# Performance work log

Measured on AMD Instinct MI355X. Metric: run time of the kernel, lower is better.

Reference implementation:

```python
import jax, jax.numpy as jnp
import numpy as np

B, M, HWIN = 1024, 5, 25          # batch, encoder window, decoder horizon
SH, SW, HID = 64, 128, 256        # saliency map H/W, hidden size
SAL = SH * SW


def setup_inputs() -> dict:
    key = jax.random.key(0)
    ks = jax.random.split(key, 32)
    s = 0.02
    W = lambda k, shp: (jax.random.normal(k, shp, jnp.float32) * s)
    inp = {
        "enc_pos": jax.random.normal(ks[0], (B, M, 3), jnp.float32),
        "enc_sal": jax.random.uniform(ks[1], (B, M, SH, SW), jnp.float32),
        "dec_pos": jax.random.normal(ks[2], (B, 1, 3), jnp.float32),
        "dec_sal": jax.random.uniform(ks[3], (B, HWIN, SH, SW), jnp.float32),
        # fc_pos_enc / fc_sal_enc
        "Wpe": W(ks[4], (3, HID)),    "bpe": W(ks[5], (HID,)),
        "Wse": W(ks[6], (SAL, HID)),  "bse": W(ks[7], (HID,)),
        # fuse_1_enc LSTM (gate order i,f,g,o like torch)
        "Wih_e": W(ks[8], (2 * HID, 4 * HID)), "Whh_e": W(ks[9], (HID, 4 * HID)),
        "bih_e": W(ks[10], (4 * HID,)),        "bhh_e": W(ks[11], (4 * HID,)),
        # fuse_1_dec LSTM
        "Wih_d": W(ks[12], (2 * HID, 4 * HID)), "Whh_d": W(ks[13], (HID, 4 * HID)),
        "bih_d": W(ks[14], (4 * HID,)),         "bhh_d": W(ks[15], (4 * HID,)),
        # fc_pos_dec / fc_sal_dec
        "Wpd": W(ks[16], (3, HID)),   "bpd": W(ks[17], (HID,)),
        "Wsd": W(ks[18], (SAL, HID)), "bsd": W(ks[19], (HID,)),
        # fuse_2 and fc_layer_out
        "W2": W(ks[20], (HID, HID)),  "b2": W(ks[21], (HID,)),
        "Wo": W(ks[22], (HID, 3)),    "bo": W(ks[23], (3,)),
    }
    return inp


def _lstm_cell(h, c, x, Wih, Whh, b):
    g = x @ Wih + h @ Whh + b                     # [B, 4H]
    i, f, gg, o = jnp.split(g, 4, axis=-1)        # torch gate order i,f,g,o
    c = jax.nn.sigmoid(f) * c + jax.nn.sigmoid(i) * jnp.tanh(gg)
    h = jax.nn.sigmoid(o) * jnp.tanh(c)
    return h, c


def reference(enc_pos, enc_sal, dec_pos, dec_sal,
              Wpe, bpe, Wse, bse, Wih_e, Whh_e, bih_e, bhh_e,
              Wih_d, Whh_d, bih_d, bhh_d, Wpd, bpd, Wsd, bsd,
              W2, b2, Wo, bo):
    b = enc_pos.shape[0]
    hid = Whh_e.shape[0]
    # ---- encoder: per-timestep linear features, then LSTM over M steps ----
    sal_e = enc_sal.reshape(b, enc_sal.shape[1], -1) @ Wse + bse   # [B,M,H]
    pos_e = enc_pos @ Wpe + bpe                                     # [B,M,H]
    x_e = jnp.concatenate([sal_e, pos_e], axis=-1)                  # [B,M,2H]
    be = bih_e + bhh_e

    h0 = jnp.zeros((b, hid), enc_pos.dtype)
    c0 = jnp.zeros((b, hid), enc_pos.dtype)

    def enc_step(carry, xt):
        h, c = carry
        h, c = _lstm_cell(h, c, xt, Wih_e, Whh_e, be)
        return (h, c), None

    (h, c), _ = jax.lax.scan(enc_step, (h0, c0), jnp.swapaxes(x_e, 0, 1))

    sal_d = dec_sal.reshape(b, dec_sal.shape[1], -1) @ Wsd + bsd    # [B,Hw,H]
    bd = bih_d + bhh_d

    def dec_step(carry, sal_t):
        h, c, pos = carry                       # pos: [B,3]
        pf = pos @ Wpd + bpd                    # fc_pos_dec
        x = jnp.concatenate([sal_t, pf], axis=-1)
        h, c = _lstm_cell(h, c, x, Wih_d, Whh_d, bd)
        delta = (h @ W2 + b2) @ Wo + bo         # fuse_2 -> fc_layer_out
        newpos = pos + delta                    # toPosition: add delta,
        newpos = newpos / jnp.linalg.norm(newpos, axis=-1, keepdims=True)
        return (h, c, newpos), newpos

    pos0 = dec_pos[:, 0, :]
    _, outs = jax.lax.scan(dec_step, (h, c, pos0), jnp.swapaxes(sal_d, 0, 1))
    return jnp.swapaxes(outs, 0, 1)             # [B, H_WINDOW, 3]
```

## Files before the change

kernel.cpp:

```cpp
#include <hip/hip_runtime.h>

typedef _Float16 f16;
typedef _Float16 f16x4 __attribute__((ext_vector_type(4)));
typedef _Float16 f16x8 __attribute__((ext_vector_type(8)));
typedef float    f32x4 __attribute__((ext_vector_type(4)));
typedef int      i32x4 __attribute__((ext_vector_type(4)));
typedef unsigned int u32;

#define MFMA16(a,b,c) __builtin_amdgcn_mfma_f32_16x16x32_f16((a),(b),(c),0,0,0)
#define MFMAI8(a,b,c) __builtin_amdgcn_mfma_i32_16x16x64_i8((a),(b),(c),0,0,0)

typedef __attribute__((address_space(1))) const u32 gu32;
typedef __attribute__((address_space(3))) u32 lu32;

static __device__ __forceinline__ float frcp(float x){ float r; asm("v_rcp_f32 %0, %1" : "=v"(r) : "v"(x)); return r; }
static __device__ __forceinline__ float frsq(float x){ float r; asm("v_rsq_f32 %0, %1" : "=v"(r) : "v"(x)); return r; }
static __device__ __forceinline__ float sigm(float x){ return frcp(1.0f + __expf(-x)); }
static __device__ __forceinline__ float tanh_(float x){ return 1.0f - 2.0f*frcp(1.0f + __expf(2.0f*x)); }

static __device__ __forceinline__ void bar_lgkm(){
  asm volatile("s_waitcnt lgkmcnt(0)" ::: "memory");
  __builtin_amdgcn_s_barrier();
  asm volatile("" ::: "memory");
}
static __device__ __forceinline__ void bar_plain(){
  asm volatile("" ::: "memory");
  __builtin_amdgcn_s_barrier();
  asm volatile("" ::: "memory");
}

static constexpr size_t OFF_WSE_P  = 0;
static constexpr size_t OFF_WSD_P  = OFF_WSE_P  + (size_t)8192*256*2;
static constexpr size_t OFF_WIHE_P = OFF_WSD_P  + (size_t)8192*256*2;
static constexpr size_t OFF_WIHD_P = OFF_WIHE_P + (size_t)256*1024*2;
static constexpr size_t OFF_WHHE_P = OFF_WIHD_P + (size_t)256*1024*2;
static constexpr size_t OFF_WHHD_P = OFF_WHHE_P + (size_t)256*1024;
static constexpr size_t OFF_W3E    = OFF_WHHD_P + (size_t)256*1024;
static constexpr size_t OFF_W3D    = OFF_W3E   + (size_t)3*1024*4;
static constexpr size_t OFF_W2WO   = OFF_W3D   + (size_t)3*1024*4;
static constexpr size_t OFF_BIASE  = OFF_W2WO  + (size_t)256*3*4;
static constexpr size_t OFF_BIASD  = OFF_BIASE + (size_t)1024*4;
static constexpr size_t OFF_B2WO   = OFF_BIASD + (size_t)1024*4;
static constexpr size_t OFF_PREGE  = OFF_B2WO  + 256;
static constexpr size_t OFF_PREGD  = OFF_PREGE + (size_t)5120*1024*2;
static constexpr size_t OFF_END    = OFF_PREGD + (size_t)25600*1024*2;

__global__ __launch_bounds__(256) void k_prep(
    const float* __restrict__ Wse, const float* __restrict__ Wsd,
    const float* __restrict__ Wih_e, const float* __restrict__ Wih_d,
    const float* __restrict__ Whh_e, const float* __restrict__ Whh_d,
    f16* pWse, f16* pWsd, f16* pWih_e, f16* pWih_d,
    signed char* pWhh_e, signed char* pWhh_d,
    const float* __restrict__ Wpe, const float* __restrict__ bpe,
    const float* __restrict__ bih_e, const float* __restrict__ bhh_e,
    const float* __restrict__ Wpd, const float* __restrict__ bpd,
    const float* __restrict__ bih_d, const float* __restrict__ bhh_d,
    const float* __restrict__ W2, const float* __restrict__ b2,
    const float* __restrict__ Wo, const float* __restrict__ bo,
    float* W3e, float* W3d, float* biasE, float* biasD, float* W2Wo, float* b2Wo)
{
  int blk = blockIdx.x;
  if (blk < 2304) {
    const float* W; f16* o; int N, base;
    if      (blk < 1024) { W=Wse;   o=pWse;   N=256;  base=0; }
    else if (blk < 2048) { W=Wsd;   o=pWsd;   N=256;  base=1024; }
    else if (blk < 2176) { W=Wih_e; o=pWih_e; N=1024; base=2048; }
    else                 { W=Wih_d; o=pWih_d; N=1024; base=2176; }
    int tid = (blk - base)*256 + threadIdx.x;
    int l = tid & 63;
    int nct = N >> 4;
    int ctg = (tid >> 6) % nct;
    int kfg = (tid >> 6) / nct;
    int k0  = kfg*32 + ((l>>4)<<3);
    int col = ctg*16 + (l&15);
    f16x8 v;
#pragma unroll
    for (int i=0;i<8;++i) v[i] = (f16)W[(size_t)(k0+i)*N + col];
    *(f16x8*)(o + (size_t)tid*8) = v;
    return;
  }
  if (blk < 2432) {
    const float* W; signed char* o; int base;
    if (blk < 2368) { W=Whh_e; o=pWhh_e; base=2304; }
    else            { W=Whh_d; o=pWhh_d; base=2368; }
    int tid = (blk - base)*256 + threadIdx.x;
    int l = tid & 63;
    int unit = tid >> 6;
    int kfg = unit >> 6, ctg = unit & 63;
    int k0  = kfg*64 + ((l>>4)<<4);
    int col = ctg*16 + (l&15);
    signed char* dst = o + ((size_t)unit*64 + l)*16;
#pragma unroll
    for (int e=0;e<16;++e) {
      int q = __float2int_rn(W[(size_t)(k0+e)*1024 + col] * 1024.0f);
      q = q > 127 ? 127 : (q < -127 ? -127 : q);
      dst[e] = (signed char)q;
    }
    return;
  }
  int bid = blk - 2432, tid = threadIdx.x;
  if (bid < 4) {
    int j = bid*256 + tid;
    float s0=0,s1=0,s2=0,sb=0;
    for (int m=0;m<256;++m) {
      float wv = Wih_e[(size_t)(256+m)*1024 + j];
      s0 += Wpe[m]*wv; s1 += Wpe[256+m]*wv; s2 += Wpe[512+m]*wv; sb += bpe[m]*wv;
    }
    W3e[j]=s0; W3e[1024+j]=s1; W3e[2048+j]=s2;
    biasE[j] = bih_e[j] + bhh_e[j] + sb;
  } else if (bid < 8) {
    int j = (bid-4)*256 + tid;
    float s0=0,s1=0,s2=0,sb=0;
    for (int m=0;m<256;++m) {
      float wv = Wih_d[(size_t)(256+m)*1024 + j];
      s0 += Wpd[m]*wv; s1 += Wpd[256+m]*wv; s2 += Wpd[512+m]*wv; sb += bpd[m]*wv;
    }
    W3d[j]=s0; W3d[1024+j]=s1; W3d[2048+j]=s2;
    biasD[j] = bih_d[j] + bhh_d[j] + sb;
  } else if (bid == 8) {
    int c = tid;
    float s0=0,s1=0,s2=0;
    for (int m=0;m<256;++m) {
      float wv = W2[(size_t)c*256+m];
      s0 += wv*Wo[m*3+0]; s1 += wv*Wo[m*3+1]; s2 += wv*Wo[m*3+2];
    }
    W2Wo[c*3+0]=s0; W2Wo[c*3+1]=s1; W2Wo[c*3+2]=s2;
  } else {
    if (tid < 192) {
      int j = tid >> 6, lane = tid & 63;
      float s = 0.f;
      for (int m=lane;m<256;m+=64) s += b2[m]*Wo[m*3+j];
#pragma unroll
      for (int msk=1;msk<64;msk<<=1) s += __shfl_xor(s, msk);
      if (lane==0) b2Wo[j] = s + bo[j];
    }
  }
}

__global__ __launch_bounds__(256) void k_gemm_fused(
    const float* __restrict__ A0, const f16* __restrict__ W0,
    const float* __restrict__ bs0, const f16* __restrict__ Wih0,
    const float* __restrict__ bias0, f16* __restrict__ P0, int nb0, int T0,
    const float* __restrict__ pos0, const float* __restrict__ W3f0,
    const float* __restrict__ A1, const f16* __restrict__ W1,
    const float* __restrict__ bs1, const f16* __restrict__ Wih1,
    const float* __restrict__ bias1, f16* __restrict__ P1, int T1)
{
  __shared__ f16 aLDS[2][64*64];
  __shared__ f16 sLDS[64*256];
  const int tid = threadIdx.x, l = tid & 63, w = tid >> 6;
  const int li = l & 15, hi = l >> 4;
  const int bx = blockIdx.x;
  const float *Ap, *bs, *bias, *posf, *W3f; const f16 *Wp, *Wih; f16* P; int rblk, T;
  if (bx < nb0) { Ap=A0; Wp=W0; bs=bs0; Wih=Wih0; bias=bias0; P=P0; rblk=bx*64;       T=T0; posf=pos0; W3f=W3f0; }
  else          { Ap=A1; Wp=W1; bs=bs1; Wih=Wih1; bias=bias1; P=P1; rblk=(bx-nb0)*64; T=T1; posf=nullptr; W3f=nullptr; }
  const int t = rblk >> 10, b0 = rblk & 1023;

  f32x4 acc[4][4];
#pragma unroll
  for (int a=0;a<4;++a)
#pragma unroll
    for (int b=0;b<4;++b) acc[a][b] = (f32x4){0.f,0.f,0.f,0.f};

  const int srow = tid >> 2, kseg = tid & 3;
  const float* Arow = Ap + ((size_t)(b0 + srow)*T + t)*8192 + kseg*16;

  float4 fA0,fA1,fA2,fA3, fB0,fB1,fB2,fB3;
#define LOADA_A(ti_) { const float* Aq = Arow + (ti_)*64;                      \
    fA0 = *(const float4*)Aq;     fA1 = *(const float4*)(Aq+4);                \
    fA2 = *(const float4*)(Aq+8); fA3 = *(const float4*)(Aq+12); }
#define LOADA_B(ti_) { const float* Aq = Arow + (ti_)*64;                      \
    fB0 = *(const float4*)Aq;     fB1 = *(const float4*)(Aq+4);                \
    fB2 = *(const float4*)(Aq+8); fB3 = *(const float4*)(Aq+12); }
#define MFMA_TILE(buf_, kfg0_)                                                 \
  _Pragma("unroll")                                                            \
  for (int kf = 0; kf < 2; ++kf) {                                             \
    f16x8 afr[4], bfr[4];                                                      \
    _Pragma("unroll")                                                          \
    for (int rt=0; rt<4; ++rt) {                                               \
      int row = rt*16 + li;                                                    \
      afr[rt] = *(f16x8*)&aLDS[buf_][row*64 + (((kf*4) + hi) ^ (row&7))*8];    \
    }                                                                          \
    _Pragma("unroll")                                                          \
    for (int ct=0; ct<4; ++ct) {                                               \
      int ctg = w*4 + ct;                                                      \
      bfr[ct] = *(const f16x8*)(Wp + ((size_t)(((kfg0_)+kf)*16 + ctg)*64 + l)*8); \
    }                                                                          \
    _Pragma("unroll")                                                          \
    for (int rt=0; rt<4; ++rt)                                                 \
      _Pragma("unroll")                                                        \
      for (int ct=0; ct<4; ++ct)                                               \
        acc[rt][ct] = MFMA16(afr[rt], bfr[ct], acc[rt][ct]);                   \
  }
#define STAGE1_STEP(F0,F1,F2,F3, RELOAD, buf_, ti_) {                          \
    f16x8 w0, w1;                                                              \
    w0[0]=(f16)F0.x; w0[1]=(f16)F0.y; w0[2]=(f16)F0.z; w0[3]=(f16)F0.w;        \
    w0[4]=(f16)F1.x; w0[5]=(f16)F1.y; w0[6]=(f16)F1.z; w0[7]=(f16)F1.w;        \
    w1[0]=(f16)F2.x; w1[1]=(f16)F2.y; w1[2]=(f16)F2.z; w1[3]=(f16)F2.w;        \
    w1[4]=(f16)F3.x; w1[5]=(f16)F3.y; w1[6]=(f16)F3.z; w1[7]=(f16)F3.w;        \
    bar_plain();                                                               \
    *(f16x8*)&aLDS[buf_][srow*64 + ((kseg*2    ) ^ (srow&7))*8] = w0;          \
    *(f16x8*)&aLDS[buf_][srow*64 + ((kseg*2 + 1) ^ (srow&7))*8] = w1;          \
    { int tn = ((ti_)+2 < 128) ? (ti_)+2 : 127; RELOAD(tn); }                  \
    bar_lgkm();                                                                \
    MFMA_TILE(buf_, (ti_)*2)                                                   \
  }

  LOADA_A(0); LOADA_B(1);
  for (int ti = 0; ti < 128; ti += 2) {
    STAGE1_STEP(fA0,fA1,fA2,fA3, LOADA_A, 0, ti)
    STAGE1_STEP(fB0,fB1,fB2,fB3, LOADA_B, 1, ti+1)
  }
#undef LOADA_A
#undef LOADA_B
#undef MFMA_TILE
#undef STAGE1_STEP
  bar_plain();
#pragma unroll
  for (int ct=0; ct<4; ++ct) {
    int col = (w*4 + ct)*16 + li;
    float bv = bs[col];
    int slot = col >> 3;
#pragma unroll
    for (int rt=0; rt<4; ++rt)
#pragma unroll
      for (int i=0;i<4;++i) {
        int row = rt*16 + hi*4 + i;
        sLDS[row*256 + ((slot ^ (row&7))<<3) + (col&7)] = (f16)(acc[rt][ct][i] + bv);
      }
  }
  float pe[4][4][3];
  if (posf) {
#pragma unroll
    for (int rt=0; rt<4; ++rt)
#pragma unroll
      for (int i=0;i<4;++i) {
        int brow = b0 + rt*16 + hi*4 + i;
        const float* pq = posf + ((size_t)brow*T + t)*3;
        pe[rt][i][0]=pq[0]; pe[rt][i][1]=pq[1]; pe[rt][i][2]=pq[2];
      }
  }
  __syncthreads();
  const int bblk0 = b0 >> 4;
#pragma unroll
  for (int cg=0; cg<4; ++cg) {
    f32x4 a2[4][4];
#pragma unroll
    for (int a=0;a<4;++a)
#pragma unroll
      for (int b=0;b<4;++b) a2[a][b] = (f32x4){0.f,0.f,0.f,0.f};
#pragma unroll
    for (int kfg=0; kfg<8; ++kfg) {
      f16x8 afr[4], bfr[4];
#pragma unroll
      for (int rt=0; rt<4; ++rt) {
        int row = rt*16 + li;
        afr[rt] = *(f16x8*)&sLDS[row*256 + (((kfg*4 + hi) ^ (row&7))<<3)];
      }
#pragma unroll
      for (int ct=0; ct<4; ++ct) {
        int ctg2 = cg*16 + w*4 + ct;
        bfr[ct] = *(const f16x8*)(Wih + ((size_t)(kfg*64 + ctg2)*64 + l)*8);
      }
#pragma unroll
      for (int rt=0; rt<4; ++rt)
#pragma unroll
        for (int ct=0; ct<4; ++ct)
          a2[rt][ct] = MFMA16(afr[rt], bfr[ct], a2[rt][ct]);
    }
#pragma unroll
    for (int ct=0; ct<4; ++ct) {
      const int ctg2 = cg*16 + w*4 + ct;
      const float bv = bias[ctg2*16 + li];
      float w30=0.f, w31=0.f, w32=0.f;
      if (posf) { int gc = ctg2*16 + li; w30=W3f[gc]; w31=W3f[1024+gc]; w32=W3f[2048+gc]; }
#pragma unroll
      for (int rt=0; rt<4; ++rt) {
        f16x4 o;
#pragma unroll
        for (int i=0;i<4;++i) {
          float v = a2[rt][ct][i] + bv;
          if (posf) v += pe[rt][i][0]*w30 + pe[rt][i][1]*w31 + pe[rt][i][2]*w32;
          o[i] = (f16)v;
        }
        *(f16x4*)(P + ((size_t)((bblk0 + rt)*T + t)*64 + ctg2)*256 + l*4) = o;
      }
    }
  }
}

__global__ __launch_bounds__(256, 1) void k_rnn(
    const f16* __restrict__ pregE,
    const f16* __restrict__ pregD,
    const signed char* __restrict__ Whh_e_p, const signed char* __restrict__ Whh_d_p,
    const float* __restrict__ W3d, const float* __restrict__ dec_pos,
    const float* __restrict__ W2Wo, const float* __restrict__ b2Wo,
    float* __restrict__ out)
{
  __shared__ signed char pLDS[4][2][16][1024];
  __shared__ signed char hBuf[2][16*256];
  __shared__ float dpart[25][16][3];
  const int tid = threadIdx.x, l = tid & 63, w = tid >> 6;
  const int li = l & 15, hi = l >> 4;
  const int bblk = blockIdx.x, rb = bblk*16;
  const float SC = 1.0f/130048.0f;

  for (int i=tid; i<25*16*3; i+=256) ((float*)dpart)[i] = 0.f;

  float c_st[4][4];
#pragma unroll
  for (int j=0;j<4;++j)
#pragma unroll
    for (int i=0;i<4;++i) c_st[j][i]=0.f;

  i32x4 wreg[32];

#define LOADWREG(WP)                                                          \
  _Pragma("unroll") for (int kk=0;kk<2;++kk)                                  \
  _Pragma("unroll") for (int f=0;f<16;++f) {                                  \
    int ctg = (f>>2)*16 + w*4 + (f&3);                                        \
    wreg[kk*16+f] = *(const i32x4*)((WP) + ((size_t)(kk*64 + ctg)*64 + l)*16); \
  }
#define LOADWLDS(WP)                                                          \
  _Pragma("unroll") for (int kk=0;kk<2;++kk)                                  \
  _Pragma("unroll") for (int f=0;f<16;++f) {                                  \
    int ctg = (f>>2)*16 + w*4 + (f&3);                                        \
    const signed char* gp = (WP) + ((size_t)((kk+2)*64 + ctg)*64 + l)*16;     \
    __builtin_amdgcn_global_load_lds((gu32*)gp, (lu32*)&pLDS[w][kk][f][0], 16, 0, 0); \
  }
#define AHK(ah, hB, kf) ah = *(i32x4*)&(hB)[li*256 + ((((kf)*4)+hi) ^ (li&7))*16];
#define MFMA_ALL(hB) {                                                        \
  i32x4 ah;                                                                   \
  _Pragma("unroll") for (int kk=0;kk<2;++kk) {                                \
    AHK(ah, hB, kk)                                                           \
    _Pragma("unroll") for (int f=0;f<16;++f)                                  \
      acc[f>>2][f&3] = MFMAI8(ah, wreg[kk*16+f], acc[f>>2][f&3]);             \
  }                                                                           \
  _Pragma("unroll") for (int kk=0;kk<2;++kk) {                                \
    AHK(ah, hB, kk+2)                                                         \
    _Pragma("unroll") for (int f=0;f<16;++f) {                                \
      i32x4 b = *(i32x4*)&pLDS[w][kk][f][l*16];                               \
      acc[f>>2][f&3] = MFMAI8(ah, b, acc[f>>2][f&3]);                         \
    }                                                                         \
  } }
#define LOADPV(dst, base, t_)                                                 \
  _Pragma("unroll")                                                           \
  for (int q=0;q<4;++q)                                                       \
    _Pragma("unroll")                                                         \
    for (int jj=0;jj<4;++jj)                                                  \
      dst[q][jj] = *(const f16x4*)((base) + ((size_t)(t_)*16384 + (size_t)(q*16 + w*4 + jj)*256 + l*4));
#define COPYPV()                                                              \
  _Pragma("unroll")                                                           \
  for (int q=0;q<4;++q)                                                       \
    _Pragma("unroll")                                                         \
    for (int jj=0;jj<4;++jj) pvA[q][jj] = pvB[q][jj];
#define ACCZERO()                                                             \
  i32x4 acc[4][4];                                                            \
  _Pragma("unroll")                                                           \
  for (int q=0;q<4;++q)                                                       \
    _Pragma("unroll")                                                         \
    for (int jj=0;jj<4;++jj) acc[q][jj] = (i32x4){0,0,0,0};
#define HWRITE(hB, r, hc, hval)                                               \
  (hB)[(r)*256 + ((((hc)>>4) ^ ((r)&7))<<4) + ((hc)&15)] =                    \
      (signed char)__float2int_rn((hval)*127.0f);
#define VMW0() { asm volatile("s_waitcnt vmcnt(0)" ::: "memory");             \
                 __builtin_amdgcn_sched_barrier(0); }

  const f16* prE = pregE + (size_t)bblk*5*16384;
  const f16* prD = pregD + (size_t)bblk*25*16384;
  f16x4 pvA[4][4], pvB[4][4];

  LOADWLDS(Whh_e_p)
  LOADWREG(Whh_e_p)
  LOADPV(pvA, prE, 0)
  VMW0()
  __syncthreads();

  for (int t=0;t<5;++t) {
    if (t+1 < 5) LOADPV(pvB, prE, t+1)
    ACCZERO()
    if (t > 0) MFMA_ALL(hBuf[(t-1)&1])
#pragma unroll
    for (int i=0;i<4;++i) {
      int r = hi*4 + i;
#pragma unroll
      for (int jj=0;jj<4;++jj) {
        int hc = w*64 + jj*16 + li;
        float gq[4];
#pragma unroll
        for (int q=0;q<4;++q)
          gq[q] = (float)pvA[q][jj][i] + (float)acc[q][jj][i]*SC;
        float cn = sigm(gq[1])*c_st[jj][i] + sigm(gq[0])*tanh_(gq[2]);
        c_st[jj][i] = cn;
        float h = sigm(gq[3])*tanh_(cn);
        HWRITE(hBuf[t&1], r, hc, h)
      }
    }
    if (t+1 < 5) { COPYPV() }
    bar_lgkm();
  }

  LOADWLDS(Whh_d_p)
  LOADWREG(Whh_d_p)
  float w3r[4][4][3];
#pragma unroll
  for (int jj=0;jj<4;++jj)
#pragma unroll
    for (int q=0;q<4;++q) {
      int gc = q*256 + w*64 + jj*16 + li;
      w3r[jj][q][0]=W3d[gc]; w3r[jj][q][1]=W3d[1024+gc]; w3r[jj][q][2]=W3d[2048+gc];
    }
  float w2r[4][3];
#pragma unroll
  for (int jj=0;jj<4;++jj) {
    int hc = w*64 + jj*16 + li;
    w2r[jj][0]=W2Wo[hc*3+0]; w2r[jj][1]=W2Wo[hc*3+1]; w2r[jj][2]=W2Wo[hc*3+2];
  }
  const float b2w0 = b2Wo[0], b2w1 = b2Wo[1], b2w2 = b2Wo[2];
  float pp[4][3];
#pragma unroll
  for (int i=0;i<4;++i) {
    int r = rb + hi*4 + i;
    pp[i][0]=dec_pos[r*3+0]; pp[i][1]=dec_pos[r*3+1]; pp[i][2]=dec_pos[r*3+2];
  }
  LOADPV(pvA, prD, 0)
  VMW0()

  for (int t=0;t<25;++t) {
    if (t+1 < 25) LOADPV(pvB, prD, t+1)
    ACCZERO()
    MFMA_ALL(hBuf[t&1])
    float dpar[4][3];
#pragma unroll
    for (int i=0;i<4;++i){ dpar[i][0]=0.f; dpar[i][1]=0.f; dpar[i][2]=0.f; }
#pragma unroll
    for (int i=0;i<4;++i) {
      int r = hi*4 + i;
#pragma unroll
      for (int jj=0;jj<4;++jj) {
        int hc = w*64 + jj*16 + li;
        float gq[4];
#pragma unroll
        for (int q=0;q<4;++q)
          gq[q] = (float)pvA[q][jj][i] + (float)acc[q][jj][i]*SC
                + pp[i][0]*w3r[jj][q][0] + pp[i][1]*w3r[jj][q][1] + pp[i][2]*w3r[jj][q][2];
        float cn = sigm(gq[1])*c_st[jj][i] + sigm(gq[0])*tanh_(gq[2]);
        c_st[jj][i] = cn;
        float h = sigm(gq[3])*tanh_(cn);
        HWRITE(hBuf[(t+1)&1], r, hc, h)
        dpar[i][0] += h*w2r[jj][0];
        dpar[i][1] += h*w2r[jj][1];
        dpar[i][2] += h*w2r[jj][2];
      }
    }
#pragma unroll
    for (int m=1;m<16;m<<=1)
#pragma unroll
      for (int i=0;i<4;++i) {
        dpar[i][0] += __shfl_xor(dpar[i][0], m);
        dpar[i][1] += __shfl_xor(dpar[i][1], m);
        dpar[i][2] += __shfl_xor(dpar[i][2], m);
      }
    if (li==0) {
#pragma unroll
      for (int i=0;i<4;++i) {
        int r = hi*4 + i;
        atomicAdd(&dpart[t][r][0], dpar[i][0]);
        atomicAdd(&dpart[t][r][1], dpar[i][1]);
        atomicAdd(&dpart[t][r][2], dpar[i][2]);
      }
    }
    if (t+1 < 25) { COPYPV() }
    bar_lgkm();
#pragma unroll
    for (int i=0;i<4;++i) {
      int r = hi*4 + i;
      float p0 = pp[i][0] + b2w0 + dpart[t][r][0];
      float p1 = pp[i][1] + b2w1 + dpart[t][r][1];
      float p2 = pp[i][2] + b2w2 + dpart[t][r][2];
      float inv = frsq(p0*p0+p1*p1+p2*p2);
      pp[i][0]=p0*inv; pp[i][1]=p1*inv; pp[i][2]=p2*inv;
      if (w==0 && li==0) {
        float* o = out + (size_t)(rb+r)*75 + t*3;
        o[0]=pp[i][0]; o[1]=pp[i][1]; o[2]=pp[i][2];
      }
    }
  }
#undef LOADWREG
#undef LOADWLDS
#undef AHK
#undef MFMA_ALL
#undef LOADPV
#undef COPYPV
#undef ACCZERO
#undef HWRITE
#undef VMW0
}

extern "C" void kernel_launch(void* const* d_in, const int* in_sizes, int n_in,
                              void* d_out, int out_size, void* d_ws, size_t ws_size,
                              hipStream_t stream)
{
  const float* enc_pos = (const float*)d_in[0];
  const float* enc_sal = (const float*)d_in[1];
  const float* dec_pos = (const float*)d_in[2];
  const float* dec_sal = (const float*)d_in[3];
  const float* Wpe  = (const float*)d_in[4];
  const float* bpe  = (const float*)d_in[5];
  const float* Wse  = (const float*)d_in[6];
  const float* bse  = (const float*)d_in[7];
  const float* Wih_e= (const float*)d_in[8];
  const float* Whh_e= (const float*)d_in[9];
  const float* bih_e= (const float*)d_in[10];
  const float* bhh_e= (const float*)d_in[11];
  const float* Wih_d= (const float*)d_in[12];
  const float* Whh_d= (const float*)d_in[13];
  const float* bih_d= (const float*)d_in[14];
  const float* bhh_d= (const float*)d_in[15];
  const float* Wpd  = (const float*)d_in[16];
  const float* bpd  = (const float*)d_in[17];
  const float* Wsd  = (const float*)d_in[18];
  const float* bsd  = (const float*)d_in[19];
  const float* W2   = (const float*)d_in[20];
  const float* b2   = (const float*)d_in[21];
  const float* Wo   = (const float*)d_in[22];
  const float* bo   = (const float*)d_in[23];

  char* ws = (char*)d_ws;
  f16* pWse   = (f16*)(ws + OFF_WSE_P);
  f16* pWsd   = (f16*)(ws + OFF_WSD_P);
  f16* pWih_e = (f16*)(ws + OFF_WIHE_P);
  f16* pWih_d = (f16*)(ws + OFF_WIHD_P);
  signed char* pWhh_e = (signed char*)(ws + OFF_WHHE_P);
  signed char* pWhh_d = (signed char*)(ws + OFF_WHHD_P);
  float* W3e  = (float*)(ws + OFF_W3E);
  float* W3d  = (float*)(ws + OFF_W3D);
  float* W2WoP= (float*)(ws + OFF_W2WO);
  float* biasE= (float*)(ws + OFF_BIASE);
  float* biasD= (float*)(ws + OFF_BIASD);
  float* b2WoP= (float*)(ws + OFF_B2WO);
  f16* pregE  = (f16*)(ws + OFF_PREGE);
  f16* pregD  = (f16*)(ws + OFF_PREGD);
  float* out  = (float*)d_out;

  hipLaunchKernelGGL(k_prep, dim3(2442), dim3(256), 0, stream,
                     Wse, Wsd, Wih_e, Wih_d, Whh_e, Whh_d,
                     pWse, pWsd, pWih_e, pWih_d, pWhh_e, pWhh_d,
                     Wpe, bpe, bih_e, bhh_e, Wpd, bpd, bih_d, bhh_d,
                     W2, b2, Wo, bo,
                     W3e, W3d, biasE, biasD, W2WoP, b2WoP);
  hipLaunchKernelGGL(k_gemm_fused, dim3(480), dim3(256), 0, stream,
                     enc_sal, pWse, bse, pWih_e, biasE, pregE, 80, 5, enc_pos, W3e,
                     dec_sal, pWsd, bsd, pWih_d, biasD, pregD, 25);
  hipLaunchKernelGGL(k_rnn, dim3(64), dim3(256), 0, stream,
                     pregE, pregD, pWhh_e, pWhh_d,
                     W3d, dec_pos, W2WoP, b2WoP, out);
}
```

Measured before the change: 522.8 us.

## Split recurrent kernel work across eight waves per block instead of four

The LSTM recurrence kernel now runs 512 threads per block. Each wave owns 32 hidden columns instead of 64, so per-wave weight registers, accumulators, preactivation buffers and LDS weight slices are halved. The goal is more latency hiding and more parallel MFMA and elementwise work on the serial recurrent critical path, with only 64 blocks in the grid. In exchange the per-step barriers now synchronise more waves and there are more atomic adds into the shared delta buffer.

```diff
diff --git a/kernel.cpp b/kernel.cpp
--- a/kernel.cpp
+++ b/kernel.cpp
@@ -289,7 +289,8 @@
   }
 }
 
-__global__ __launch_bounds__(256, 1) void k_rnn(
+__global__ __launch_bounds__(512) __attribute__((amdgpu_waves_per_eu(2,2)))
+void k_rnn(
     const f16* __restrict__ pregE,
     const f16* __restrict__ pregD,
     const signed char* __restrict__ Whh_e_p, const signed char* __restrict__ Whh_d_p,
@@ -297,7 +298,7 @@
     const float* __restrict__ W2Wo, const float* __restrict__ b2Wo,
     float* __restrict__ out)
 {
-  __shared__ signed char pLDS[4][2][16][1024];
+  __shared__ signed char pLDS[8][2][8][1024];
   __shared__ signed char hBuf[2][16*256];
   __shared__ float dpart[25][16][3];
   const int tid = threadIdx.x, l = tid & 63, w = tid >> 6;
@@ -305,26 +306,26 @@
   const int bblk = blockIdx.x, rb = bblk*16;
   const float SC = 1.0f/130048.0f;
 
-  for (int i=tid; i<25*16*3; i+=256) ((float*)dpart)[i] = 0.f;
-
-  float c_st[4][4];
-#pragma unroll
-  for (int j=0;j<4;++j)
+  for (int i=tid; i<25*16*3; i+=512) ((float*)dpart)[i] = 0.f;
+
+  float c_st[2][4];
+#pragma unroll
+  for (int j=0;j<2;++j)
 #pragma unroll
     for (int i=0;i<4;++i) c_st[j][i]=0.f;
 
-  i32x4 wreg[32];
+  i32x4 wreg[16];
 
 #define LOADWREG(WP)                                                          \
   _Pragma("unroll") for (int kk=0;kk<2;++kk)                                  \
-  _Pragma("unroll") for (int f=0;f<16;++f) {                                  \
-    int ctg = (f>>2)*16 + w*4 + (f&3);                                        \
-    wreg[kk*16+f] = *(const i32x4*)((WP) + ((size_t)(kk*64 + ctg)*64 + l)*16); \
+  _Pragma("unroll") for (int f=0;f<8;++f) {                                   \
+    int ctg = (f>>1)*16 + w*2 + (f&1);                                        \
+    wreg[kk*8+f] = *(const i32x4*)((WP) + ((size_t)(kk*64 + ctg)*64 + l)*16); \
   }
 #define LOADWLDS(WP)                                                          \
   _Pragma("unroll") for (int kk=0;kk<2;++kk)                                  \
-  _Pragma("unroll") for (int f=0;f<16;++f) {                                  \
-    int ctg = (f>>2)*16 + w*4 + (f&3);                                        \
+  _Pragma("unroll") for (int f=0;f<8;++f) {                                   \
+    int ctg = (f>>1)*16 + w*2 + (f&1);                                        \
     const signed char* gp = (WP) + ((size_t)((kk+2)*64 + ctg)*64 + l)*16;     \
     __builtin_amdgcn_global_load_lds((gu32*)gp, (lu32*)&pLDS[w][kk][f][0], 16, 0, 0); \
   }
@@ -333,33 +334,33 @@
   i32x4 ah;                                                                   \
   _Pragma("unroll") for (int kk=0;kk<2;++kk) {                                \
     AHK(ah, hB, kk)                                                           \
-    _Pragma("unroll") for (int f=0;f<16;++f)                                  \
-      acc[f>>2][f&3] = MFMAI8(ah, wreg[kk*16+f], acc[f>>2][f&3]);             \
+    _Pragma("unroll") for (int f=0;f<8;++f)                                   \
+      acc[f>>1][f&1] = MFMAI8(ah, wreg[kk*8+f], acc[f>>1][f&1]);              \
   }                                                                           \
   _Pragma("unroll") for (int kk=0;kk<2;++kk) {                                \
     AHK(ah, hB, kk+2)                                                         \
-    _Pragma("unroll") for (int f=0;f<16;++f) {                                \
+    _Pragma("unroll") for (int f=0;f<8;++f) {                                 \
       i32x4 b = *(i32x4*)&pLDS[w][kk][f][l*16];                               \
-      acc[f>>2][f&3] = MFMAI8(ah, b, acc[f>>2][f&3]);                         \
+      acc[f>>1][f&1] = MFMAI8(ah, b, acc[f>>1][f&1]);                         \
     }                                                                         \
   } }
 #define LOADPV(dst, base, t_)                                                 \
   _Pragma("unroll")                                                           \
   for (int q=0;q<4;++q)                                                       \
     _Pragma("unroll")                                                         \
-    for (int jj=0;jj<4;++jj)                                                  \
-      dst[q][jj] = *(const f16x4*)((base) + ((size_t)(t_)*16384 + (size_t)(q*16 + w*4 + jj)*256 + l*4));
+    for (int j=0;j<2;++j)                                                     \
+      dst[q][j] = *(const f16x4*)((base) + ((size_t)(t_)*16384 + (size_t)(q*16 + w*2 + j)*256 + l*4));
 #define COPYPV()                                                              \
   _Pragma("unroll")                                                           \
   for (int q=0;q<4;++q)                                                       \
     _Pragma("unroll")                                                         \
-    for (int jj=0;jj<4;++jj) pvA[q][jj] = pvB[q][jj];
+    for (int j=0;j<2;++j) pvA[q][j] = pvB[q][j];
 #define ACCZERO()                                                             \
-  i32x4 acc[4][4];                                                            \
+  i32x4 acc[4][2];                                                            \
   _Pragma("unroll")                                                           \
   for (int q=0;q<4;++q)                                                       \
     _Pragma("unroll")                                                         \
-    for (int jj=0;jj<4;++jj) acc[q][jj] = (i32x4){0,0,0,0};
+    for (int j=0;j<2;++j) acc[q][j] = (i32x4){0,0,0,0};
 #define HWRITE(hB, r, hc, hval)                                               \
   (hB)[(r)*256 + ((((hc)>>4) ^ ((r)&7))<<4) + ((hc)&15)] =                    \
       (signed char)__float2int_rn((hval)*127.0f);
@@ -368,7 +369,7 @@
 
   const f16* prE = pregE + (size_t)bblk*5*16384;
   const f16* prD = pregD + (size_t)bblk*25*16384;
-  f16x4 pvA[4][4], pvB[4][4];
+  f16x4 pvA[4][2], pvB[4][2];
 
   LOADWLDS(Whh_e_p)
   LOADWREG(Whh_e_p)
@@ -384,14 +385,14 @@
     for (int i=0;i<4;++i) {
       int r = hi*4 + i;
 #pragma unroll
-      for (int jj=0;jj<4;++jj) {
-        int hc = w*64 + jj*16 + li;
+      for (int j=0;j<2;++j) {
+        int hc = w*32 + j*16 + li;
         float gq[4];
 #pragma unroll
         for (int q=0;q<4;++q)
-          gq[q] = (float)pvA[q][jj][i] + (float)acc[q][jj][i]*SC;
-        float cn = sigm(gq[1])*c_st[jj][i] + sigm(gq[0])*tanh_(gq[2]);
-        c_st[jj][i] = cn;
+          gq[q] = (float)pvA[q][j][i] + (float)acc[q][j][i]*SC;
+        float cn = sigm(gq[1])*c_st[j][i] + sigm(gq[0])*tanh_(gq[2]);
+        c_st[j][i] = cn;
         float h = sigm(gq[3])*tanh_(cn);
         HWRITE(hBuf[t&1], r, hc, h)
       }
@@ -402,19 +403,19 @@
 
   LOADWLDS(Whh_d_p)
   LOADWREG(Whh_d_p)
-  float w3r[4][4][3];
-#pragma unroll
-  for (int jj=0;jj<4;++jj)
+  float w3r[2][4][3];
+#pragma unroll
+  for (int j=0;j<2;++j)
 #pragma unroll
     for (int q=0;q<4;++q) {
-      int gc = q*256 + w*64 + jj*16 + li;
-      w3r[jj][q][0]=W3d[gc]; w3r[jj][q][1]=W3d[1024+gc]; w3r[jj][q][2]=W3d[2048+gc];
-    }
-  float w2r[4][3];
-#pragma unroll
-  for (int jj=0;jj<4;++jj) {
-    int hc = w*64 + jj*16 + li;
-    w2r[jj][0]=W2Wo[hc*3+0]; w2r[jj][1]=W2Wo[hc*3+1]; w2r[jj][2]=W2Wo[hc*3+2];
+      int gc = q*256 + w*32 + j*16 + li;
+      w3r[j][q][0]=W3d[gc]; w3r[j][q][1]=W3d[1024+gc]; w3r[j][q][2]=W3d[2048+gc];
+    }
+  float w2r[2][3];
+#pragma unroll
+  for (int j=0;j<2;++j) {
+    int hc = w*32 + j*16 + li;
+    w2r[j][0]=W2Wo[hc*3+0]; w2r[j][1]=W2Wo[hc*3+1]; w2r[j][2]=W2Wo[hc*3+2];
   }
   const float b2w0 = b2Wo[0], b2w1 = b2Wo[1], b2w2 = b2Wo[2];
   float pp[4][3];
@@ -437,20 +438,20 @@
     for (int i=0;i<4;++i) {
       int r = hi*4 + i;
 #pragma unroll
-      for (int jj=0;jj<4;++jj) {
-        int hc = w*64 + jj*16 + li;
+      for (int j=0;j<2;++j) {
+        int hc = w*32 + j*16 + li;
         float gq[4];
 #pragma unroll
         for (int q=0;q<4;++q)
-          gq[q] = (float)pvA[q][jj][i] + (float)acc[q][jj][i]*SC
-                + pp[i][0]*w3r[jj][q][0] + pp[i][1]*w3r[jj][q][1] + pp[i][2]*w3r[jj][q][2];
-        float cn = sigm(gq[1])*c_st[jj][i] + sigm(gq[0])*tanh_(gq[2]);
-        c_st[jj][i] = cn;
+          gq[q] = (float)pvA[q][j][i] + (float)acc[q][j][i]*SC
+                + pp[i][0]*w3r[j][q][0] + pp[i][1]*w3r[j][q][1] + pp[i][2]*w3r[j][q][2];
+        float cn = sigm(gq[1])*c_st[j][i] + sigm(gq[0])*tanh_(gq[2]);
+        c_st[j][i] = cn;
         float h = sigm(gq[3])*tanh_(cn);
         HWRITE(hBuf[(t+1)&1], r, hc, h)
-        dpar[i][0] += h*w2r[jj][0];
-        dpar[i][1] += h*w2r[jj][1];
-        dpar[i][2] += h*w2r[jj][2];
+        dpar[i][0] += h*w2r[j][0];
+        dpar[i][1] += h*w2r[j][1];
+        dpar[i][2] += h*w2r[j][2];
       }
     }
 #pragma unroll
@@ -552,7 +553,7 @@
   hipLaunchKernelGGL(k_gemm_fused, dim3(480), dim3(256), 0, stream,
                      enc_sal, pWse, bse, pWih_e, biasE, pregE, 80, 5, enc_pos, W3e,
                      dec_sal, pWsd, bsd, pWih_d, biasD, pregD, 25);
-  hipLaunchKernelGGL(k_rnn, dim3(64), dim3(256), 0, stream,
+  hipLaunchKernelGGL(k_rnn, dim3(64), dim3(512), 0, stream,
                      pregE, pregD, pWhh_e, pWhh_d,
                      W3d, dec_pos, W2WoP, b2WoP, out);
 }
```

Result: faster. 480.1 us (-8.2%).

## Spread recurrent LSTM kernel over 16 waves per block instead of 4

Applied to the files above, without the earlier changes.

The recurrent kernel now runs 1024 threads (16 wavefronts) per batch block, with each wave owning one 16-column hidden slice instead of four. Per-thread MFMA, register and gate work drops fourfold, which shortens the serial per-timestep critical path. The W3 position weights are staged in LDS as fp16, and the preactivation prefetch double-buffering is removed. The tradeoffs are unhidden global loads at the start of each timestep, more waves taking part in each barrier, and fp16 rounding of W3.

```diff
diff --git a/kernel.cpp b/kernel.cpp
--- a/kernel.cpp
+++ b/kernel.cpp
@@ -289,7 +289,7 @@
   }
 }
 
-__global__ __launch_bounds__(256, 1) void k_rnn(
+__global__ __launch_bounds__(1024) void k_rnn(
     const f16* __restrict__ pregE,
     const f16* __restrict__ pregD,
     const signed char* __restrict__ Whh_e_p, const signed char* __restrict__ Whh_d_p,
@@ -297,69 +297,60 @@
     const float* __restrict__ W2Wo, const float* __restrict__ b2Wo,
     float* __restrict__ out)
 {
-  __shared__ signed char pLDS[4][2][16][1024];
+  __shared__ signed char pLDS[16][2][4][1024];
   __shared__ signed char hBuf[2][16*256];
+  __shared__ f16 W3h[3*1024];
   __shared__ float dpart[25][16][3];
   const int tid = threadIdx.x, l = tid & 63, w = tid >> 6;
   const int li = l & 15, hi = l >> 4;
   const int bblk = blockIdx.x, rb = bblk*16;
   const float SC = 1.0f/130048.0f;
 
-  for (int i=tid; i<25*16*3; i+=256) ((float*)dpart)[i] = 0.f;
-
-  float c_st[4][4];
-#pragma unroll
-  for (int j=0;j<4;++j)
-#pragma unroll
-    for (int i=0;i<4;++i) c_st[j][i]=0.f;
-
-  i32x4 wreg[32];
+  for (int i=tid;i<3072;i+=1024) W3h[i] = (f16)W3d[i];
+  for (int i=tid; i<25*16*3; i+=1024) ((float*)dpart)[i] = 0.f;
+
+  float c_st[4];
+#pragma unroll
+  for (int i=0;i<4;++i) c_st[i]=0.f;
+
+  i32x4 wreg[8];
 
 #define LOADWREG(WP)                                                          \
   _Pragma("unroll") for (int kk=0;kk<2;++kk)                                  \
-  _Pragma("unroll") for (int f=0;f<16;++f) {                                  \
-    int ctg = (f>>2)*16 + w*4 + (f&3);                                        \
-    wreg[kk*16+f] = *(const i32x4*)((WP) + ((size_t)(kk*64 + ctg)*64 + l)*16); \
+  _Pragma("unroll") for (int q=0;q<4;++q) {                                   \
+    int ctg = q*16 + w;                                                       \
+    wreg[kk*4+q] = *(const i32x4*)((WP) + ((size_t)(kk*64 + ctg)*64 + l)*16); \
   }
 #define LOADWLDS(WP)                                                          \
   _Pragma("unroll") for (int kk=0;kk<2;++kk)                                  \
-  _Pragma("unroll") for (int f=0;f<16;++f) {                                  \
-    int ctg = (f>>2)*16 + w*4 + (f&3);                                        \
+  _Pragma("unroll") for (int q=0;q<4;++q) {                                   \
+    int ctg = q*16 + w;                                                       \
     const signed char* gp = (WP) + ((size_t)((kk+2)*64 + ctg)*64 + l)*16;     \
-    __builtin_amdgcn_global_load_lds((gu32*)gp, (lu32*)&pLDS[w][kk][f][0], 16, 0, 0); \
+    __builtin_amdgcn_global_load_lds((gu32*)gp, (lu32*)&pLDS[w][kk][q][0], 16, 0, 0); \
   }
 #define AHK(ah, hB, kf) ah = *(i32x4*)&(hB)[li*256 + ((((kf)*4)+hi) ^ (li&7))*16];
 #define MFMA_ALL(hB) {                                                        \
   i32x4 ah;                                                                   \
   _Pragma("unroll") for (int kk=0;kk<2;++kk) {                                \
     AHK(ah, hB, kk)                                                           \
-    _Pragma("unroll") for (int f=0;f<16;++f)                                  \
-      acc[f>>2][f&3] = MFMAI8(ah, wreg[kk*16+f], acc[f>>2][f&3]);             \
+    _Pragma("unroll") for (int q=0;q<4;++q)                                   \
+      acc[q] = MFMAI8(ah, wreg[kk*4+q], acc[q]);                              \
   }                                                                           \
   _Pragma("unroll") for (int kk=0;kk<2;++kk) {                                \
     AHK(ah, hB, kk+2)                                                         \
-    _Pragma("unroll") for (int f=0;f<16;++f) {                                \
-      i32x4 b = *(i32x4*)&pLDS[w][kk][f][l*16];                               \
-      acc[f>>2][f&3] = MFMAI8(ah, b, acc[f>>2][f&3]);                         \
+    _Pragma("unroll") for (int q=0;q<4;++q) {                                 \
+      i32x4 b = *(i32x4*)&pLDS[w][kk][q][l*16];                               \
+      acc[q] = MFMAI8(ah, b, acc[q]);                                         \
     }                                                                         \
   } }
 #define LOADPV(dst, base, t_)                                                 \
   _Pragma("unroll")                                                           \
   for (int q=0;q<4;++q)                                                       \
-    _Pragma("unroll")                                                         \
-    for (int jj=0;jj<4;++jj)                                                  \
-      dst[q][jj] = *(const f16x4*)((base) + ((size_t)(t_)*16384 + (size_t)(q*16 + w*4 + jj)*256 + l*4));
-#define COPYPV()                                                              \
+    dst[q] = *(const f16x4*)((base) + ((size_t)(t_)*16384 + (size_t)(q*16 + w)*256 + l*4));
+#define ACCZERO()                                                             \
+  i32x4 acc[4];                                                               \
   _Pragma("unroll")                                                           \
-  for (int q=0;q<4;++q)                                                       \
-    _Pragma("unroll")                                                         \
-    for (int jj=0;jj<4;++jj) pvA[q][jj] = pvB[q][jj];
-#define ACCZERO()                                                             \
-  i32x4 acc[4][4];                                                            \
-  _Pragma("unroll")                                                           \
-  for (int q=0;q<4;++q)                                                       \
-    _Pragma("unroll")                                                         \
-    for (int jj=0;jj<4;++jj) acc[q][jj] = (i32x4){0,0,0,0};
+  for (int q=0;q<4;++q) acc[q] = (i32x4){0,0,0,0};
 #define HWRITE(hB, r, hc, hval)                                               \
   (hB)[(r)*256 + ((((hc)>>4) ^ ((r)&7))<<4) + ((hc)&15)] =                    \
       (signed char)__float2int_rn((hval)*127.0f);
@@ -368,54 +359,37 @@
 
   const f16* prE = pregE + (size_t)bblk*5*16384;
   const f16* prD = pregD + (size_t)bblk*25*16384;
-  f16x4 pvA[4][4], pvB[4][4];
+  const int hc = w*16 + li;
+  f16x4 pvA[4];
 
   LOADWLDS(Whh_e_p)
   LOADWREG(Whh_e_p)
-  LOADPV(pvA, prE, 0)
   VMW0()
   __syncthreads();
 
   for (int t=0;t<5;++t) {
-    if (t+1 < 5) LOADPV(pvB, prE, t+1)
+    LOADPV(pvA, prE, t)
     ACCZERO()
     if (t > 0) MFMA_ALL(hBuf[(t-1)&1])
 #pragma unroll
     for (int i=0;i<4;++i) {
       int r = hi*4 + i;
-#pragma unroll
-      for (int jj=0;jj<4;++jj) {
-        int hc = w*64 + jj*16 + li;
-        float gq[4];
-#pragma unroll
-        for (int q=0;q<4;++q)
-          gq[q] = (float)pvA[q][jj][i] + (float)acc[q][jj][i]*SC;
-        float cn = sigm(gq[1])*c_st[jj][i] + sigm(gq[0])*tanh_(gq[2]);
-        c_st[jj][i] = cn;
-        float h = sigm(gq[3])*tanh_(cn);
-        HWRITE(hBuf[t&1], r, hc, h)
-      }
-    }
-    if (t+1 < 5) { COPYPV() }
+      float gq[4];
+#pragma unroll
+      for (int q=0;q<4;++q)
+        gq[q] = (float)pvA[q][i] + (float)acc[q][i]*SC;
+      float cn = sigm(gq[1])*c_st[i] + sigm(gq[0])*tanh_(gq[2]);
+      c_st[i] = cn;
+      float h = sigm(gq[3])*tanh_(cn);
+      HWRITE(hBuf[t&1], r, hc, h)
+    }
     bar_lgkm();
   }
 
   LOADWLDS(Whh_d_p)
   LOADWREG(Whh_d_p)
-  float w3r[4][4][3];
-#pragma unroll
-  for (int jj=0;jj<4;++jj)
-#pragma unroll
-    for (int q=0;q<4;++q) {
-      int gc = q*256 + w*64 + jj*16 + li;
-      w3r[jj][q][0]=W3d[gc]; w3r[jj][q][1]=W3d[1024+gc]; w3r[jj][q][2]=W3d[2048+gc];
-    }
-  float w2r[4][3];
-#pragma unroll
-  for (int jj=0;jj<4;++jj) {
-    int hc = w*64 + jj*16 + li;
-    w2r[jj][0]=W2Wo[hc*3+0]; w2r[jj][1]=W2Wo[hc*3+1]; w2r[jj][2]=W2Wo[hc*3+2];
-  }
+  float w2r[3];
+  w2r[0]=W2Wo[hc*3+0]; w2r[1]=W2Wo[hc*3+1]; w2r[2]=W2Wo[hc*3+2];
   const float b2w0 = b2Wo[0], b2w1 = b2Wo[1], b2w2 = b2Wo[2];
   float pp[4][3];
 #pragma unroll
@@ -423,35 +397,36 @@
     int r = rb + hi*4 + i;
     pp[i][0]=dec_pos[r*3+0]; pp[i][1]=dec_pos[r*3+1]; pp[i][2]=dec_pos[r*3+2];
   }
-  LOADPV(pvA, prD, 0)
   VMW0()
 
   for (int t=0;t<25;++t) {
-    if (t+1 < 25) LOADPV(pvB, prD, t+1)
+    LOADPV(pvA, prD, t)
     ACCZERO()
     MFMA_ALL(hBuf[t&1])
+    float w3v[4][3];
+#pragma unroll
+    for (int q=0;q<4;++q) {
+      int gc = q*256 + hc;
+      w3v[q][0] = (float)W3h[gc];
+      w3v[q][1] = (float)W3h[1024+gc];
+      w3v[q][2] = (float)W3h[2048+gc];
+    }
     float dpar[4][3];
-#pragma unroll
-    for (int i=0;i<4;++i){ dpar[i][0]=0.f; dpar[i][1]=0.f; dpar[i][2]=0.f; }
 #pragma unroll
     for (int i=0;i<4;++i) {
       int r = hi*4 + i;
-#pragma unroll
-      for (int jj=0;jj<4;++jj) {
-        int hc = w*64 + jj*16 + li;
-        float gq[4];
-#pragma unroll
-        for (int q=0;q<4;++q)
-          gq[q] = (float)pvA[q][jj][i] + (float)acc[q][jj][i]*SC
-                + pp[i][0]*w3r[jj][q][0] + pp[i][1]*w3r[jj][q][1] + pp[i][2]*w3r[jj][q][2];
-        float cn = sigm(gq[1])*c_st[jj][i] + sigm(gq[0])*tanh_(gq[2]);
-        c_st[jj][i] = cn;
-        float h = sigm(gq[3])*tanh_(cn);
-        HWRITE(hBuf[(t+1)&1], r, hc, h)
-        dpar[i][0] += h*w2r[jj][0];
-        dpar[i][1] += h*w2r[jj][1];
-        dpar[i][2] += h*w2r[jj][2];
-      }
+      float gq[4];
+#pragma unroll
+      for (int q=0;q<4;++q)
+        gq[q] = (float)pvA[q][i] + (float)acc[q][i]*SC
+              + pp[i][0]*w3v[q][0] + pp[i][1]*w3v[q][1] + pp[i][2]*w3v[q][2];
+      float cn = sigm(gq[1])*c_st[i] + sigm(gq[0])*tanh_(gq[2]);
+      c_st[i] = cn;
+      float h = sigm(gq[3])*tanh_(cn);
+      HWRITE(hBuf[(t+1)&1], r, hc, h)
+      dpar[i][0] = h*w2r[0];
+      dpar[i][1] = h*w2r[1];
+      dpar[i][2] = h*w2r[2];
     }
 #pragma unroll
     for (int m=1;m<16;m<<=1)
@@ -470,7 +445,6 @@
         atomicAdd(&dpart[t][r][2], dpar[i][2]);
       }
     }
-    if (t+1 < 25) { COPYPV() }
     bar_lgkm();
 #pragma unroll
     for (int i=0;i<4;++i) {
@@ -491,7 +465,6 @@
 #undef AHK
 #undef MFMA_ALL
 #undef LOADPV
-#undef COPYPV
 #undef ACCZERO
 #undef HWRITE
 #undef VMW0
@@ -552,7 +525,7 @@
   hipLaunchKernelGGL(k_gemm_fused, dim3(480), dim3(256), 0, stream,
                      enc_sal, pWse, bse, pWih_e, biasE, pregE, 80, 5, enc_pos, W3e,
                      dec_sal, pWsd, bsd, pWih_d, biasD, pregD, 25);
-  hipLaunchKernelGGL(k_rnn, dim3(64), dim3(256), 0, stream,
+  hipLaunchKernelGGL(k_rnn, dim3(64), dim3(1024), 0, stream,
                      pregE, pregD, pWhh_e, pWhh_d,
                      W3d, dec_pos, W2WoP, b2WoP, out);
 }
```

Measured after the change: 475.2 us (median of 2 runs). 9.1% less time.
